# Performance work log

Hardware: AMD Instinct MI355X
Metric: run time of the kernel (lower is better)

Reference implementation:

```python
import jax, jax.numpy as jnp
import numpy as np

BETA = 0.25  # commitment_cost


def setup_inputs() -> dict:
    key = jax.random.key(0)
    k1, k2 = jax.random.split(key)
    B, T, D, K = 16, 2048, 512, 4096
    z_e = jax.random.normal(k1, (B, T, D), dtype=jnp.float32)
    # torch init is uniform(-1/K, 1/K); use normal scaled similarly for a nontrivial codebook
    codebook = jax.random.normal(k2, (K, D), dtype=jnp.float32) * (1.0 / K)
    return {"z_e": z_e, "codebook": codebook}


def reference(z_e, codebook):
    B, T, D = z_e.shape
    K = codebook.shape[0]
    x = z_e.reshape(B * T, D)  # [N, D]
    distances = (
        jnp.sum(x * x, axis=1, keepdims=True)
        - 2.0 * (x @ codebook.T)
        + jnp.sum(codebook * codebook, axis=1)
    )
    k = jnp.argmin(distances, axis=1)  # [N] int
    z_q = codebook[k]  # [N, D] gather
    # straight-through estimator
    z_q_st = x + jax.lax.stop_gradient(z_q - x)
    # use_ema=True branch: vq_loss = beta * mse(z_e, detach(z_q))
    commitment_loss = jnp.mean(jnp.square(x - jax.lax.stop_gradient(z_q)))
    vq_loss = BETA * commitment_loss
    # utilization = number of unique codes / K (jit-friendly via scatter)
    used = jnp.zeros((K,), dtype=jnp.float32).at[k].set(1.0)
    utilization = jnp.sum(used) / K
    return (z_q_st.reshape(B, T, D), k.reshape(B, T), vq_loss, utilization)
```

## Files before the change

### kernel.cpp

```cpp
#include <hip/hip_runtime.h>
#include <hip/hip_bf16.h>


typedef _Float16 half8 __attribute__((ext_vector_type(8)));
typedef float floatx4 __attribute__((ext_vector_type(4)));
typedef unsigned long long u64;

#define N_ROWS 32768
#define DDIM   512
#define KCODES 4096
#define SCALE  1024.0f
#define SCALE2 1048576.0f
#define TAUK   (250u << 12)
#define BIASF  524288.0f
#define PAIR_CAP 8192
#define FULL_CAP 1024
#define LOSS_BLOCKS 8192

#define WH_OFF   0u
#define WSQS_OFF (4u*1024u*1024u)
#define SWW_OFF  (WSQS_OFF + 16384u)
#define SXX_OFF  (SWW_OFF + 16384u)
#define ST_K1    (SXX_OFF + 131072u)
#define ST_K2    (ST_K1 + 262144u)
#define ST_K3    (ST_K2 + 262144u)
#define IDX_OFF  (ST_K3 + 262144u)
#define PROW_OFF (IDX_OFF + 131072u)
#define PIDS_OFF (PROW_OFF + 4u*PAIR_CAP)
#define FROW_OFF (PIDS_OFF + 4u*PAIR_CAP)
#define FRES_OFF (FROW_OFF + 4u*FULL_CAP)
#define PCNT_OFF (FRES_OFF + 8u*FULL_CAP)
#define FCNT_OFF (PCNT_OFF + 256u)
#define LPART_OFF (FCNT_OFF + 256u)
#define USED_OFF (LPART_OFF + 4u*LOSS_BLOCKS)

__device__ __forceinline__ unsigned fkey(float f) {
    unsigned u = __float_as_uint(f);
    return (u & 0x80000000u) ? ~u : (u | 0x80000000u);
}

__device__ __forceinline__ float np_d32(float sxx, float dot32, float sww) {
    float t = sxx - 2.0f * dot32;
    return t + sww;
}

__device__ __forceinline__ unsigned uminu(unsigned a, unsigned b) { return a < b ? a : b; }
__device__ __forceinline__ unsigned umaxu(unsigned a, unsigned b) { return a > b ? a : b; }

__device__ __forceinline__ unsigned med3u(unsigned a, unsigned b, unsigned c) {
    unsigned r;
    asm("v_med3_u32 %0, %1, %2, %3" : "=v"(r) : "v"(a), "v"(b), "v"(c));
    return r;
}

typedef const __attribute__((address_space(1))) void* as1cv;
typedef __attribute__((address_space(3))) void* as3v;
__device__ __forceinline__ void gld_lds16(const void* g, void* l) {
    __builtin_amdgcn_global_load_lds((as1cv)g, (as3v)l, 16, 0, 0);
}

__global__ void k0_init(unsigned* used, unsigned* pcnt, unsigned* fcnt, u64* fres) {
    int t = threadIdx.x;
    for (int i = t; i < KCODES; i += 256) used[i] = 0u;
    for (int i = t; i < FULL_CAP; i += 256) fres[i] = ~0ull;
    if (t == 0) { *pcnt = 0u; *fcnt = 0u; }
}

__global__ void k1_convert(const float* __restrict__ w, half8* __restrict__ wh) {
    int u = blockIdx.x * 256 + threadIdx.x;
    int b = u >> 10, rem = u & 1023, c = rem >> 6, q = (rem >> 4) & 3, ri = rem & 15;
    int row = b * 16 + ri, d0 = c * 32 + q * 8;
    const float* p = w + (size_t)row * DDIM + d0;
    half8 h;
#pragma unroll
    for (int e = 0; e < 8; ++e) h[e] = (_Float16)(p[e] * SCALE);
    wh[u] = h;
}

__global__ void k1b_wsq(const float* __restrict__ w, float* __restrict__ wsqs,
                        float* __restrict__ sww) {
    int lane = threadIdx.x & 63;
    int wave = blockIdx.x * 4 + (threadIdx.x >> 6);
    for (int k = wave; k < KCODES; k += 256) {
        const float* p = w + (size_t)k * DDIM;
        double s = 0.0;
#pragma unroll
        for (int m = 0; m < 8; ++m) { double v = p[lane + m * 64]; s += v * v; }
#pragma unroll
        for (int m = 1; m < 64; m <<= 1) s += __shfl_xor(s, m, 64);
        if (lane == 0) {
            sww[k]  = (float)s;
            wsqs[k] = (float)(s * (double)SCALE2);
        }
    }
}

__global__ void k1c_sxx(const float* __restrict__ x, float* __restrict__ sxx) {
#pragma clang fp contract(off)
    int lane = threadIdx.x & 63;
    int row = blockIdx.x * 4 + (threadIdx.x >> 6);
    if (row >= N_ROWS) return;
    const float* p = x + (size_t)row * DDIM;
    int b = (lane >> 3) & 3, j = lane & 7;
    const float* q = p + b * 128 + j;
    float v0 = q[0];
    float s = v0 * v0;
#pragma unroll
    for (int i = 1; i < 16; ++i) { float v = q[8 * i]; float m = v * v; s = s + m; }
    s = s + __shfl_xor(s, 1, 64);
    s = s + __shfl_xor(s, 2, 64);
    s = s + __shfl_xor(s, 4, 64);
    s = s + __shfl_xor(s, 8, 64);
    s = s + __shfl_xor(s, 16, 64);
    if (lane == 0) sxx[row] = s;
}

__launch_bounds__(256, 2)
__global__ void k2_main(const float* __restrict__ x, const half8* __restrict__ wh,
                        const float* __restrict__ wsqs,
                        unsigned* __restrict__ sK1, unsigned* __restrict__ sK2,
                        unsigned* __restrict__ sK3) {
    __shared__ half8 w_lds[2][2048];
    __shared__ float wsq_lds[2048];
    const int tid  = threadIdx.x;
    const int lane = tid & 63;
    const int wv   = tid >> 6;
    const int ks   = blockIdx.x & 1;
    const int rt   = blockIdx.x >> 1;
    const int r0   = rt * 128 + wv * 32;
    const int col  = lane & 15;
    const int q    = lane >> 4;

    for (int i = tid; i < 2048; i += 256) wsq_lds[i] = wsqs[ks * 2048 + i] + BIASF;

    half8 a[2][16];
#pragma unroll
    for (int i = 0; i < 2; ++i) {
        int row = r0 + i * 16 + col;
        const float* xr = x + (size_t)row * DDIM + q * 8;
#pragma unroll
        for (int c = 0; c < 16; ++c) {
            const float4* xp = (const float4*)(xr + c * 32);
            float4 lo = xp[0], hi = xp[1];
            half8 h;
            h[0]=(_Float16)lo.x; h[1]=(_Float16)lo.y; h[2]=(_Float16)lo.z; h[3]=(_Float16)lo.w;
            h[4]=(_Float16)hi.x; h[5]=(_Float16)hi.y; h[6]=(_Float16)hi.z; h[7]=(_Float16)hi.w;
            a[i][c] = h;
        }
    }

    unsigned K1[8], K2[8], K3[8];
#pragma unroll
    for (int j = 0; j < 8; ++j) { K1[j] = ~0u; K2[j] = ~0u; K3[j] = ~0u; }

    const half8* wbase = wh + (size_t)ks * 131072;

#pragma unroll
    for (int j = 0; j < 8; ++j)
        gld_lds16(wbase + j * 256 + tid, &w_lds[0][j * 256 + wv * 64]);
    __syncthreads();

    for (int ph = 0; ph < 64; ++ph) {
        const int buf = ph & 1;
        if (ph < 63) {
            const half8* gph = wbase + (size_t)(ph + 1) * 2048;
#pragma unroll
            for (int j = 0; j < 8; ++j)
                gld_lds16(gph + j * 256 + tid, &w_lds[buf ^ 1][j * 256 + wv * 64]);
        }
        floatx4 acc00 = {0.f,0.f,0.f,0.f}, acc01 = {0.f,0.f,0.f,0.f};
        floatx4 acc10 = {0.f,0.f,0.f,0.f}, acc11 = {0.f,0.f,0.f,0.f};
        __builtin_amdgcn_s_setprio(1);
#pragma unroll
        for (int c = 0; c < 16; ++c) {
            half8 b0 = w_lds[buf][c * 64 + lane];
            half8 b1 = w_lds[buf][1024 + c * 64 + lane];
            acc00 = __builtin_amdgcn_mfma_f32_16x16x32_f16(a[0][c], b0, acc00, 0, 0, 0);
            acc10 = __builtin_amdgcn_mfma_f32_16x16x32_f16(a[1][c], b0, acc10, 0, 0, 0);
            acc01 = __builtin_amdgcn_mfma_f32_16x16x32_f16(a[0][c], b1, acc01, 0, 0, 0);
            acc11 = __builtin_amdgcn_mfma_f32_16x16x32_f16(a[1][c], b1, acc11, 0, 0, 0);
        }
        __builtin_amdgcn_s_setprio(0);
        __syncthreads();

        const int cb = (ph << 5) + col;
        const unsigned code0 = (unsigned)(ks * 2048 + cb);
        const unsigned code1 = code0 + 16u;
        const float w0 = wsq_lds[cb];
        const float w1 = wsq_lds[cb + 16];
#pragma unroll
        for (int r = 0; r < 4; ++r) {
            {
                float s0 = fmaf(-2048.0f, acc00[r], w0);
                unsigned key0 = ((unsigned)s0 << 12) | code0;
                unsigned n1 = uminu(K1[r], key0);
                unsigned n2 = med3u(K1[r], K2[r], key0);
                unsigned n3 = med3u(K2[r], K3[r], key0);
                float s1 = fmaf(-2048.0f, acc01[r], w1);
                unsigned key1 = ((unsigned)s1 << 12) | code1;
                K1[r] = uminu(n1, key1);
                K2[r] = med3u(n1, n2, key1);
                K3[r] = med3u(n2, n3, key1);
            }
            {
                int j = 4 + r;
                float s0 = fmaf(-2048.0f, acc10[r], w0);
                unsigned key0 = ((unsigned)s0 << 12) | code0;
                unsigned n1 = uminu(K1[j], key0);
                unsigned n2 = med3u(K1[j], K2[j], key0);
                unsigned n3 = med3u(K2[j], K3[j], key0);
                float s1 = fmaf(-2048.0f, acc11[r], w1);
                unsigned key1 = ((unsigned)s1 << 12) | code1;
                K1[j] = uminu(n1, key1);
                K2[j] = med3u(n1, n2, key1);
                K3[j] = med3u(n2, n3, key1);
            }
        }
    }

#pragma unroll
    for (int j = 0; j < 8; ++j) {
        unsigned a1 = K1[j], a2 = K2[j], a3 = K3[j];
#pragma unroll
        for (int mask = 1; mask <= 8; mask <<= 1) {
            unsigned b1 = (unsigned)__shfl_xor((int)a1, mask, 64);
            unsigned b2 = (unsigned)__shfl_xor((int)a2, mask, 64);
            unsigned b3 = (unsigned)__shfl_xor((int)a3, mask, 64);
            unsigned r1 = uminu(a1, b1);
            unsigned r2 = uminu(umaxu(a1, b1), uminu(a2, b2));
            unsigned r3 = uminu(uminu(umaxu(a2, b1), umaxu(a1, b2)), uminu(a3, b3));
            a1 = r1; a2 = r2; a3 = r3;
        }
        if (col == 0) {
            int row = r0 + (j >> 2) * 16 + q * 4 + (j & 3);
            size_t o = (size_t)ks * N_ROWS + row;
            sK1[o] = a1; sK2[o] = a2; sK3[o] = a3;
        }
    }
}

__global__ void k3_merge(const unsigned* __restrict__ sK1, const unsigned* __restrict__ sK2,
                         const unsigned* __restrict__ sK3,
                         int* __restrict__ idxArr, float* __restrict__ outk,
                         unsigned* __restrict__ pRow, unsigned* __restrict__ pIds,
                         unsigned* __restrict__ pCnt,
                         unsigned* __restrict__ fRow, unsigned* __restrict__ fCnt) {
    int row = blockIdx.x * 256 + threadIdx.x;
    unsigned a1 = sK1[row], a2 = sK2[row], a3 = sK3[row];
    unsigned b1 = sK1[N_ROWS + row], b2 = sK2[N_ROWS + row], b3 = sK3[N_ROWS + row];
    unsigned r1 = uminu(a1, b1);
    unsigned r2 = uminu(umaxu(a1, b1), uminu(a2, b2));
    unsigned r3 = uminu(uminu(umaxu(a2, b1), umaxu(a1, b2)), uminu(a3, b3));
    int i1 = (int)(r1 & 4095u);
    idxArr[row] = i1;
    outk[row] = (float)i1;
    if (r3 - r1 < TAUK) {
        unsigned p = atomicAdd(fCnt, 1u);
        if (p < FULL_CAP) fRow[p] = (unsigned)row;
    } else if (r2 - r1 < TAUK) {
        unsigned p = atomicAdd(pCnt, 1u);
        if (p < PAIR_CAP) {
            pRow[p] = (unsigned)row;
            pIds[p] = (r1 & 4095u) | ((r2 & 4095u) << 16);
        }
    }
}

__global__ void k4p_pair(const float* __restrict__ x, const float* __restrict__ w,
                         const float* __restrict__ sww, const float* __restrict__ sxx,
                         const unsigned* __restrict__ pRow, const unsigned* __restrict__ pIds,
                         const unsigned* __restrict__ pCnt,
                         int* __restrict__ idxArr, float* __restrict__ outk) {
    int n = (int)*pCnt; if (n > PAIR_CAP) n = PAIR_CAP;
    const int lane = threadIdx.x & 63;
    const int wave = blockIdx.x * 4 + (threadIdx.x >> 6);
    for (int i = wave; i < n; i += 512) {
        int row = (int)pRow[i] & (N_ROWS - 1);
        unsigned ids = pIds[i];
        int i1 = (int)(ids & 0xFFFFu) & (KCODES - 1);
        int i2 = (int)(ids >> 16) & (KCODES - 1);
        const float* xp = x + (size_t)row * DDIM;
        int code = (lane < 32) ? i1 : i2;
        const float* wp = w + (size_t)code * DDIM;
        int l32 = lane & 31;
        double dt = 0.0;
#pragma unroll
        for (int m = 0; m < 16; ++m) {
            int d = l32 + 32 * m;
            dt += (double)xp[d] * (double)wp[d];
        }
#pragma unroll
        for (int m = 1; m <= 16; m <<= 1) dt += __shfl_xor(dt, m, 64);
        double dot1 = __shfl(dt, 0, 64);
        double dot2 = __shfl(dt, 32, 64);
        if (lane == 0) {
            float sxx32 = sxx[row];
            float d1 = np_d32(sxx32, (float)dot1, sww[i1]);
            float d2 = np_d32(sxx32, (float)dot2, sww[i2]);
            bool take2 = (d2 < d1) || (d2 == d1 && i2 < i1);
            if (take2) { idxArr[row] = i2; outk[row] = (float)i2; }
        }
    }
}

__launch_bounds__(256, 4)
__global__ void k4f_full(const float* __restrict__ x, const float* __restrict__ w,
                         const float* __restrict__ sww, const float* __restrict__ sxx,
                         const unsigned* __restrict__ fRow, const unsigned* __restrict__ fCnt,
                         u64* __restrict__ fRes) {
    __shared__ int rws[4];
    __shared__ u64 sred[4];
    int n = (int)*fCnt; if (n > FULL_CAP) n = FULL_CAP;
    const int t = threadIdx.x, lane = t & 63, wv = t >> 6;
    const int slice = blockIdx.x & 15, slot0 = blockIdx.x >> 4;
    for (int g = slot0; g * 4 < n; g += 64) {
        if (t < 4) {
            int fi = g * 4 + t;
            rws[t] = (int)fRow[fi < n ? fi : (n - 1)] & (N_ROWS - 1);
            sred[t] = ~0ull;
        }
        __syncthreads();
        float xv[4][8];
        float sxxs[4];
#pragma unroll
        for (int r = 0; r < 4; ++r) {
            const float* xp = x + (size_t)rws[r] * DDIM;
#pragma unroll
            for (int m = 0; m < 8; ++m) xv[r][m] = xp[lane + 64 * m];
            sxxs[r] = sxx[rws[r]];
        }
        for (int cc = 0; cc < 64; ++cc) {
            int code = slice * 256 + wv * 64 + cc;
            const float* wp = w + (size_t)code * DDIM;
            float dt[4];
#pragma unroll
            for (int r = 0; r < 4; ++r) dt[r] = 0.f;
#pragma unroll
            for (int m = 0; m < 8; ++m) {
                float wvv = wp[lane + 64 * m];
#pragma unroll
                for (int r = 0; r < 4; ++r) dt[r] = fmaf(wvv, xv[r][m], dt[r]);
            }
#pragma unroll
            for (int r = 0; r < 4; ++r) {
#pragma unroll
                for (int mask = 1; mask < 64; mask <<= 1) dt[r] += __shfl_xor(dt[r], mask, 64);
            }
            if (lane == 0) {
                float swwc = sww[code];
#pragma unroll
                for (int r = 0; r < 4; ++r) {
                    float dd = np_d32(sxxs[r], dt[r], swwc);
                    u64 pk = ((u64)fkey(dd) << 32) | (unsigned)code;
                    atomicMin(&sred[r], pk);
                }
            }
        }
        __syncthreads();
        if (t < 4) {
            int fi = g * 4 + t;
            if (fi < n) atomicMin(&fRes[fi], sred[t]);
        }
        __syncthreads();
    }
}

__global__ void k4g_write(const unsigned* __restrict__ fRow, const unsigned* __restrict__ fCnt,
                          const u64* __restrict__ fRes,
                          int* __restrict__ idxArr, float* __restrict__ outk) {
    int n = (int)*fCnt; if (n > FULL_CAP) n = FULL_CAP;
    for (int fi = threadIdx.x; fi < n; fi += 256) {
        int row = (int)fRow[fi] & (N_ROWS - 1);
        int code = (int)(unsigned)(fRes[fi] & 0xFFFFFFFFull) & (KCODES - 1);
        idxArr[row] = code;
        outk[row] = (float)code;
    }
}

__global__ void k5_gather(const float* __restrict__ x, const float* __restrict__ w,
                          const int* __restrict__ idxArr, float* __restrict__ outzq,
                          unsigned* __restrict__ used, float* __restrict__ lossPart) {
    __shared__ float lred[4];
    int g = blockIdx.x * 256 + threadIdx.x;
    int row = g >> 6, c8 = g & 63;
    int idx = idxArr[row] & (KCODES - 1);
    const float4* cb = (const float4*)(w + (size_t)idx * DDIM + c8 * 8);
    const float4* xp = (const float4*)(x + (size_t)row * DDIM + c8 * 8);
    float4* zq = (float4*)(outzq + (size_t)row * DDIM + c8 * 8);
    float4 c0 = cb[0], c1 = cb[1];
    float4 x0 = xp[0], x1 = xp[1];
    zq[0] = c0; zq[1] = c1;
    float part = 0.f;
    float d;
    d = x0.x - c0.x; part = fmaf(d, d, part);
    d = x0.y - c0.y; part = fmaf(d, d, part);
    d = x0.z - c0.z; part = fmaf(d, d, part);
    d = x0.w - c0.w; part = fmaf(d, d, part);
    d = x1.x - c1.x; part = fmaf(d, d, part);
    d = x1.y - c1.y; part = fmaf(d, d, part);
    d = x1.z - c1.z; part = fmaf(d, d, part);
    d = x1.w - c1.w; part = fmaf(d, d, part);
    if (c8 == 0) used[idx] = 1u;
#pragma unroll
    for (int m = 1; m < 64; m <<= 1) part += __shfl_xor(part, m, 64);
    int wv = threadIdx.x >> 6;
    if ((threadIdx.x & 63) == 0) lred[wv] = part;
    __syncthreads();
    if (threadIdx.x == 0)
        lossPart[blockIdx.x] = (lred[0] + lred[1]) + (lred[2] + lred[3]);
}

__global__ void k6_final(const unsigned* __restrict__ used, const float* __restrict__ lossPart,
                         float* __restrict__ out) {
    __shared__ int sred[256];
    __shared__ float fred[256];
    int t = threadIdx.x;
    int s = 0;
    for (int i = t; i < KCODES; i += 256) s += (int)used[i];
    float ls = 0.f;
    for (int i = t; i < LOSS_BLOCKS; i += 256) ls += lossPart[i];
    sred[t] = s; fred[t] = ls; __syncthreads();
    for (int off = 128; off > 0; off >>= 1) {
        if (t < off) { sred[t] += sred[t + off]; fred[t] += fred[t + off]; }
        __syncthreads();
    }
    if (t == 0) {
        size_t base = (size_t)N_ROWS * DDIM + N_ROWS;
        out[base]     = 0.25f * fred[0] / 16777216.0f;
        out[base + 1] = (float)sred[0] / 4096.0f;
    }
}

extern "C" void kernel_launch(void* const* d_in, const int* in_sizes, int n_in,
                              void* d_out, int out_size, void* d_ws, size_t ws_size,
                              hipStream_t stream) {
    (void)in_sizes; (void)n_in; (void)out_size; (void)ws_size;
    const float* x = (const float*)d_in[0];
    const float* w = (const float*)d_in[1];
    float* out = (float*)d_out;
    char* ws = (char*)d_ws;

    half8*    wh   = (half8*)(ws + WH_OFF);
    float*    wsqs = (float*)(ws + WSQS_OFF);
    float*    sww  = (float*)(ws + SWW_OFF);
    float*    sxx  = (float*)(ws + SXX_OFF);
    unsigned* sK1  = (unsigned*)(ws + ST_K1);
    unsigned* sK2  = (unsigned*)(ws + ST_K2);
    unsigned* sK3  = (unsigned*)(ws + ST_K3);
    int*      idxA = (int*)(ws + IDX_OFF);
    unsigned* pRow = (unsigned*)(ws + PROW_OFF);
    unsigned* pIds = (unsigned*)(ws + PIDS_OFF);
    unsigned* fRow = (unsigned*)(ws + FROW_OFF);
    u64*      fRes = (u64*)(ws + FRES_OFF);
    unsigned* pCnt = (unsigned*)(ws + PCNT_OFF);
    unsigned* fCnt = (unsigned*)(ws + FCNT_OFF);
    float*    lPart= (float*)(ws + LPART_OFF);
    unsigned* used = (unsigned*)(ws + USED_OFF);

    float* outk = out + (size_t)N_ROWS * DDIM;

    k0_init<<<1, 256, 0, stream>>>(used, pCnt, fCnt, fRes);
    k1_convert<<<1024, 256, 0, stream>>>(w, wh);
    k1b_wsq<<<64, 256, 0, stream>>>(w, wsqs, sww);
    k1c_sxx<<<8192, 256, 0, stream>>>(x, sxx);
    k2_main<<<512, 256, 0, stream>>>(x, wh, wsqs, sK1, sK2, sK3);
    k3_merge<<<128, 256, 0, stream>>>(sK1, sK2, sK3, idxA, outk,
                                      pRow, pIds, pCnt, fRow, fCnt);
    k4p_pair<<<128, 256, 0, stream>>>(x, w, sww, sxx, pRow, pIds, pCnt, idxA, outk);
    k4f_full<<<1024, 256, 0, stream>>>(x, w, sww, sxx, fRow, fCnt, fRes);
    k4g_write<<<1, 256, 0, stream>>>(fRow, fCnt, fRes, idxA, outk);
    k5_gather<<<8192, 256, 0, stream>>>(x, w, idxA, out, used, lPart);
    k6_final<<<1, 256, 0, stream>>>(used, lPart, out);
}
```

Measured before the change: 398.3 us.

## Enlarge k2_main tiles to 64 rows per wave and 64 codes per phase

Each wave now holds 64 rows of x (4 row tiles) in registers instead of 32, and each phase stages 64 codes into LDS instead of 32. This halves the grid to 256 blocks, one per CU, and halves the number of phases and barriers. Every LDS-loaded B fragment now feeds four MFMAs instead of two. The top-3 update is also interleaved per column tile rather than done after all MFMAs. In exchange, register pressure roughly doubles (A fragments plus 48 top-3 registers) and occupancy drops to one block per CU, which risks spills and less latency hiding. The 256-block grid may also under-fill the device.

```diff
diff --git a/kernel.cpp b/kernel.cpp
--- a/kernel.cpp
+++ b/kernel.cpp
@@ -115,28 +115,34 @@
     if (lane == 0) sxx[row] = s;
 }
 
-__launch_bounds__(256, 2)
+__launch_bounds__(256, 1)
 __global__ void k2_main(const float* __restrict__ x, const half8* __restrict__ wh,
                         const float* __restrict__ wsqs,
                         unsigned* __restrict__ sK1, unsigned* __restrict__ sK2,
                         unsigned* __restrict__ sK3) {
-    __shared__ half8 w_lds[2][2048];
+    __shared__ half8 w_lds[2][4096];
     __shared__ float wsq_lds[2048];
     const int tid  = threadIdx.x;
     const int lane = tid & 63;
     const int wv   = tid >> 6;
     const int ks   = blockIdx.x & 1;
-    const int rt   = blockIdx.x >> 1;
-    const int r0   = rt * 128 + wv * 32;
+    const int rb   = blockIdx.x >> 1;
+    const int R0   = rb * 256 + wv * 64;
     const int col  = lane & 15;
     const int q    = lane >> 4;
 
+    const half8* wbase = wh + (size_t)ks * 131072;
+
+#pragma unroll
+    for (int j = 0; j < 16; ++j)
+        gld_lds16(wbase + j * 256 + tid, &w_lds[0][j * 256 + wv * 64]);
+
     for (int i = tid; i < 2048; i += 256) wsq_lds[i] = wsqs[ks * 2048 + i] + BIASF;
 
-    half8 a[2][16];
-#pragma unroll
-    for (int i = 0; i < 2; ++i) {
-        int row = r0 + i * 16 + col;
+    half8 a[4][16];
+#pragma unroll
+    for (int rt = 0; rt < 4; ++rt) {
+        int row = R0 + rt * 16 + col;
         const float* xr = x + (size_t)row * DDIM + q * 8;
 #pragma unroll
         for (int c = 0; c < 16; ++c) {
@@ -145,81 +151,75 @@
             half8 h;
             h[0]=(_Float16)lo.x; h[1]=(_Float16)lo.y; h[2]=(_Float16)lo.z; h[3]=(_Float16)lo.w;
             h[4]=(_Float16)hi.x; h[5]=(_Float16)hi.y; h[6]=(_Float16)hi.z; h[7]=(_Float16)hi.w;
-            a[i][c] = h;
-        }
-    }
-
-    unsigned K1[8], K2[8], K3[8];
-#pragma unroll
-    for (int j = 0; j < 8; ++j) { K1[j] = ~0u; K2[j] = ~0u; K3[j] = ~0u; }
-
-    const half8* wbase = wh + (size_t)ks * 131072;
-
-#pragma unroll
-    for (int j = 0; j < 8; ++j)
-        gld_lds16(wbase + j * 256 + tid, &w_lds[0][j * 256 + wv * 64]);
+            a[rt][c] = h;
+        }
+    }
+
+    unsigned K1[16], K2[16], K3[16];
+#pragma unroll
+    for (int j = 0; j < 16; ++j) { K1[j] = ~0u; K2[j] = ~0u; K3[j] = ~0u; }
+
     __syncthreads();
 
-    for (int ph = 0; ph < 64; ++ph) {
+    for (int ph = 0; ph < 32; ++ph) {
         const int buf = ph & 1;
-        if (ph < 63) {
-            const half8* gph = wbase + (size_t)(ph + 1) * 2048;
-#pragma unroll
-            for (int j = 0; j < 8; ++j)
+        if (ph < 31) {
+            const half8* gph = wbase + (size_t)(ph + 1) * 4096;
+#pragma unroll
+            for (int j = 0; j < 16; ++j)
                 gld_lds16(gph + j * 256 + tid, &w_lds[buf ^ 1][j * 256 + wv * 64]);
         }
-        floatx4 acc00 = {0.f,0.f,0.f,0.f}, acc01 = {0.f,0.f,0.f,0.f};
-        floatx4 acc10 = {0.f,0.f,0.f,0.f}, acc11 = {0.f,0.f,0.f,0.f};
-        __builtin_amdgcn_s_setprio(1);
-#pragma unroll
-        for (int c = 0; c < 16; ++c) {
-            half8 b0 = w_lds[buf][c * 64 + lane];
-            half8 b1 = w_lds[buf][1024 + c * 64 + lane];
-            acc00 = __builtin_amdgcn_mfma_f32_16x16x32_f16(a[0][c], b0, acc00, 0, 0, 0);
-            acc10 = __builtin_amdgcn_mfma_f32_16x16x32_f16(a[1][c], b0, acc10, 0, 0, 0);
-            acc01 = __builtin_amdgcn_mfma_f32_16x16x32_f16(a[0][c], b1, acc01, 0, 0, 0);
-            acc11 = __builtin_amdgcn_mfma_f32_16x16x32_f16(a[1][c], b1, acc11, 0, 0, 0);
-        }
-        __builtin_amdgcn_s_setprio(0);
+#pragma unroll
+        for (int ct = 0; ct < 4; ++ct) {
+            floatx4 acc0 = {0.f,0.f,0.f,0.f}, acc1 = {0.f,0.f,0.f,0.f};
+            floatx4 acc2 = {0.f,0.f,0.f,0.f}, acc3 = {0.f,0.f,0.f,0.f};
+#pragma unroll
+            for (int kc = 0; kc < 16; ++kc) {
+                half8 b = w_lds[buf][ct * 1024 + kc * 64 + lane];
+                acc0 = __builtin_amdgcn_mfma_f32_16x16x32_f16(a[0][kc], b, acc0, 0, 0, 0);
+                acc1 = __builtin_amdgcn_mfma_f32_16x16x32_f16(a[1][kc], b, acc1, 0, 0, 0);
+                acc2 = __builtin_amdgcn_mfma_f32_16x16x32_f16(a[2][kc], b, acc2, 0, 0, 0);
+                acc3 = __builtin_amdgcn_mfma_f32_16x16x32_f16(a[3][kc], b, acc3, 0, 0, 0);
+            }
+            const int cb = (ph << 6) + (ct << 4) + col;
+            const unsigned code = (unsigned)(ks * 2048) + (unsigned)cb;
+            const float wq = wsq_lds[cb];
+#pragma unroll
+            for (int r = 0; r < 4; ++r) {
+                {   float s = fmaf(-2048.0f, acc0[r], wq);
+                    unsigned key = ((unsigned)s << 12) | code;
+                    unsigned n1 = uminu(K1[r], key);
+                    unsigned n2 = med3u(K1[r], K2[r], key);
+                    unsigned n3 = med3u(K2[r], K3[r], key);
+                    K1[r] = n1; K2[r] = n2; K3[r] = n3; }
+                {   int j = 4 + r;
+                    float s = fmaf(-2048.0f, acc1[r], wq);
+                    unsigned key = ((unsigned)s << 12) | code;
+                    unsigned n1 = uminu(K1[j], key);
+                    unsigned n2 = med3u(K1[j], K2[j], key);
+                    unsigned n3 = med3u(K2[j], K3[j], key);
+                    K1[j] = n1; K2[j] = n2; K3[j] = n3; }
+                {   int j = 8 + r;
+                    float s = fmaf(-2048.0f, acc2[r], wq);
+                    unsigned key = ((unsigned)s << 12) | code;
+                    unsigned n1 = uminu(K1[j], key);
+                    unsigned n2 = med3u(K1[j], K2[j], key);
+                    unsigned n3 = med3u(K2[j], K3[j], key);
+                    K1[j] = n1; K2[j] = n2; K3[j] = n3; }
+                {   int j = 12 + r;
+                    float s = fmaf(-2048.0f, acc3[r], wq);
+                    unsigned key = ((unsigned)s << 12) | code;
+                    unsigned n1 = uminu(K1[j], key);
+                    unsigned n2 = med3u(K1[j], K2[j], key);
+                    unsigned n3 = med3u(K2[j], K3[j], key);
+                    K1[j] = n1; K2[j] = n2; K3[j] = n3; }
+            }
+        }
         __syncthreads();
-
-        const int cb = (ph << 5) + col;
-        const unsigned code0 = (unsigned)(ks * 2048 + cb);
-        const unsigned code1 = code0 + 16u;
-        const float w0 = wsq_lds[cb];
-        const float w1 = wsq_lds[cb + 16];
-#pragma unroll
-        for (int r = 0; r < 4; ++r) {
-            {
-                float s0 = fmaf(-2048.0f, acc00[r], w0);
-                unsigned key0 = ((unsigned)s0 << 12) | code0;
-                unsigned n1 = uminu(K1[r], key0);
-                unsigned n2 = med3u(K1[r], K2[r], key0);
-                unsigned n3 = med3u(K2[r], K3[r], key0);
-                float s1 = fmaf(-2048.0f, acc01[r], w1);
-                unsigned key1 = ((unsigned)s1 << 12) | code1;
-                K1[r] = uminu(n1, key1);
-                K2[r] = med3u(n1, n2, key1);
-                K3[r] = med3u(n2, n3, key1);
-            }
-            {
-                int j = 4 + r;
-                float s0 = fmaf(-2048.0f, acc10[r], w0);
-                unsigned key0 = ((unsigned)s0 << 12) | code0;
-                unsigned n1 = uminu(K1[j], key0);
-                unsigned n2 = med3u(K1[j], K2[j], key0);
-                unsigned n3 = med3u(K2[j], K3[j], key0);
-                float s1 = fmaf(-2048.0f, acc11[r], w1);
-                unsigned key1 = ((unsigned)s1 << 12) | code1;
-                K1[j] = uminu(n1, key1);
-                K2[j] = med3u(n1, n2, key1);
-                K3[j] = med3u(n2, n3, key1);
-            }
-        }
-    }
-
-#pragma unroll
-    for (int j = 0; j < 8; ++j) {
+    }
+
+#pragma unroll
+    for (int j = 0; j < 16; ++j) {
         unsigned a1 = K1[j], a2 = K2[j], a3 = K3[j];
 #pragma unroll
         for (int mask = 1; mask <= 8; mask <<= 1) {
@@ -232,7 +232,7 @@
             a1 = r1; a2 = r2; a3 = r3;
         }
         if (col == 0) {
-            int row = r0 + (j >> 2) * 16 + q * 4 + (j & 3);
+            int row = R0 + (j >> 2) * 16 + q * 4 + (j & 3);
             size_t o = (size_t)ks * N_ROWS + row;
             sK1[o] = a1; sK2[o] = a2; sK3[o] = a3;
         }
@@ -463,7 +463,7 @@
     k1_convert<<<1024, 256, 0, stream>>>(w, wh);
     k1b_wsq<<<64, 256, 0, stream>>>(w, wsqs, sww);
     k1c_sxx<<<8192, 256, 0, stream>>>(x, sxx);
-    k2_main<<<512, 256, 0, stream>>>(x, wh, wsqs, sK1, sK2, sK3);
+    k2_main<<<256, 256, 0, stream>>>(x, wh, wsqs, sK1, sK2, sK3);
     k3_merge<<<128, 256, 0, stream>>>(sK1, sK2, sK3, idxA, outk,
                                       pRow, pIds, pCnt, fRow, fCnt);
     k4p_pair<<<128, 256, 0, stream>>>(x, w, sww, sxx, pRow, pIds, pCnt, idxA, outk);
```

Measured after the change: 444.4 us. +11.6%, slower.
